# Kernel optimization log

Measured on AMD Instinct MI355X. Metric: run time of the kernel, lower is better.

## Reference

```python
import jax, jax.numpy as jnp
import numpy as np

B, S, H, NH = 2, 2048, 1024, 16
HD = H // NH  # 64
SCALE = HD ** -0.5


def setup_inputs() -> dict:
    key = jax.random.key(0)
    k1, k2, k3 = jax.random.split(key, 3)
    x = jax.random.normal(k1, (B, S, H), dtype=jnp.float32)
    w_qkv = jax.random.normal(k2, (H, 3 * H), dtype=jnp.float32) * (H ** -0.5)
    b_qkv = jnp.zeros((3 * H,), dtype=jnp.float32)
    w_out = jax.random.normal(k3, (H, H), dtype=jnp.float32) * (H ** -0.5)
    b_out = jnp.zeros((H,), dtype=jnp.float32)
    return {"x": x, "w_qkv": w_qkv, "b_qkv": b_qkv, "w_out": w_out, "b_out": b_out}


def reference(x, w_qkv, b_qkv, w_out, b_out):
    # qkv projection: [B,S,3H] -> split -> [B,NH,S,HD] each
    qkv = x @ w_qkv + b_qkv
    q, k, v = jnp.split(qkv, 3, axis=-1)
    def heads(t):
        return t.reshape(B, S, NH, HD).transpose(0, 2, 1, 3)  # [B,NH,S,HD]
    q, k, v = heads(q), heads(k), heads(v)
    # full (non-causal) softmax attention; chunking in the original is
    # math-equivalent since each query row attends over all keys
    scores = jnp.einsum('bhqd,bhkd->bhqk', q, k) * SCALE
    attn = jax.nn.softmax(scores, axis=-1)
    out = jnp.einsum('bhqk,bhkd->bhqd', attn, v)  # [B,NH,S,HD]
    out = out.transpose(0, 2, 1, 3).reshape(B, S, H)
    # to_out linear (Dropout is identity in eval mode)
    return out @ w_out + b_out
```

## Files before the change

### kernel.cpp

```cpp
#include <hip/hip_runtime.h>
#include <cstdint>

using u16 = unsigned short;
typedef __bf16 bf16x8 __attribute__((ext_vector_type(8)));
typedef __bf16 bf16x4 __attribute__((ext_vector_type(4)));
typedef float f32x4 __attribute__((ext_vector_type(4)));

#define MFMA16(a, b, c) __builtin_amdgcn_mfma_f32_16x16x32_bf16((a), (b), (c), 0, 0, 0)

__device__ __forceinline__ u16 f2bf(float f) {
  union { float f; uint32_t u; } c; c.f = f;
  uint32_t u = c.u;
  u += 0x7fffu + ((u >> 16) & 1u);
  return (u16)(u >> 16);
}

#if __has_builtin(__builtin_amdgcn_global_load_lds)
#define GLOAD_LDS16(g, l)                                                      \
  __builtin_amdgcn_global_load_lds(                                            \
      (__attribute__((address_space(1))) void*)(g),                            \
      (__attribute__((address_space(3))) void*)(l), 16, 0, 0)
#else
#define GLOAD_LDS16(g, l) do { *(uint4*)(l) = *(const uint4*)(g); } while (0)
#endif

__global__ __launch_bounds__(256) void prep(
    const float* __restrict__ x, const float* __restrict__ w_qkv,
    const float* __restrict__ w_out, u16* __restrict__ xb,
    u16* __restrict__ wqT, u16* __restrict__ woT) {
  const int bid = blockIdx.x, tid = threadIdx.x;
  if (bid < 4096) {
    int i = (bid * 256 + tid) * 4;
    float4 v = *(const float4*)&x[i];
    ushort4 p;
    p.x = f2bf(v.x); p.y = f2bf(v.y); p.z = f2bf(v.z); p.w = f2bf(v.w);
    *(ushort4*)&xb[i] = p;
    return;
  }
  __shared__ float tile[32][33];
  int t = bid - 4096;
  const float* in;
  u16* outp;
  int C, bx, by;
  if (t < 3072) { in = w_qkv; outp = wqT; C = 3072; bx = (t % 96) * 32; by = (t / 96) * 32; }
  else { t -= 3072; in = w_out; outp = woT; C = 1024; bx = (t % 32) * 32; by = (t / 32) * 32; }
  const int R = 1024;
  const int tx = tid & 31, ty = tid >> 5;
#pragma unroll
  for (int r2 = 0; r2 < 4; ++r2)
    tile[ty + r2 * 8][tx] = in[(size_t)(by + ty + r2 * 8) * C + bx + tx];
  __syncthreads();
#pragma unroll
  for (int r2 = 0; r2 < 4; ++r2)
    outp[(size_t)(bx + ty + r2 * 8) * R + by + tx] = f2bf(tile[tx][ty + r2 * 8]);
}

__global__ __launch_bounds__(256, 2) void gemm_qkv(
    const u16* __restrict__ A, const u16* __restrict__ Bt,
    const float* __restrict__ bias,
    u16* __restrict__ qb, u16* __restrict__ kb, u16* __restrict__ vb,
    int M, int N, int K) {
  __shared__ u16 As[128 * 32];
  __shared__ u16 Bs[128 * 32];
  const int tid = threadIdx.x;
  const int m0 = blockIdx.x * 128;
  const int n0 = blockIdx.y * 128;
  const int lane = tid & 63, w = tid >> 6;
  const int quad = lane >> 4, l16 = lane & 15;
  const int wr = w >> 1, wc = w & 1;

  f32x4 acc[4][4] = {};

  const int r0 = tid >> 2, p0 = tid & 3;
  const int r1 = r0 + 64;
  const int c8 = p0 ^ ((r0 >> 1) & 3);
  const u16* ga0 = A + (size_t)(m0 + r0) * K + c8 * 8;
  const u16* ga1 = A + (size_t)(m0 + r1) * K + c8 * 8;
  const u16* gb0 = Bt + (size_t)(n0 + r0) * K + c8 * 8;
  const u16* gb1 = Bt + (size_t)(n0 + r1) * K + c8 * 8;
  u16* la0 = &As[tid * 8];
  u16* la1 = &As[(tid + 256) * 8];
  u16* lb0 = &Bs[tid * 8];
  u16* lb1 = &Bs[(tid + 256) * 8];

  int aoff[4], boff[4];
#pragma unroll
  for (int i = 0; i < 4; ++i) {
    int ra = wr * 64 + i * 16 + l16;
    aoff[i] = (ra * 4 + (quad ^ ((ra >> 1) & 3))) * 8;
    int rb = wc * 64 + i * 16 + l16;
    boff[i] = (rb * 4 + (quad ^ ((rb >> 1) & 3))) * 8;
  }

  const int nIter = K >> 5;
  for (int kt = 0; kt < nIter; ++kt) {
    __syncthreads();
    const int kk = kt << 5;
    GLOAD_LDS16(ga0 + kk, la0);
    GLOAD_LDS16(ga1 + kk, la1);
    GLOAD_LDS16(gb0 + kk, lb0);
    GLOAD_LDS16(gb1 + kk, lb1);
    __syncthreads();
    bf16x8 af[4], bfr[4];
#pragma unroll
    for (int i = 0; i < 4; ++i) af[i] = *(const bf16x8*)&As[aoff[i]];
#pragma unroll
    for (int j = 0; j < 4; ++j) bfr[j] = *(const bf16x8*)&Bs[boff[j]];
#pragma unroll
    for (int i = 0; i < 4; ++i)
#pragma unroll
      for (int j = 0; j < 4; ++j)
        acc[i][j] = MFMA16(af[i], bfr[j], acc[i][j]);
  }

  const int S = 2048, NH = 16;
#pragma unroll
  for (int i = 0; i < 4; ++i) {
    const int mb = m0 + wr * 64 + i * 16 + quad * 4;
#pragma unroll
    for (int j = 0; j < 4; ++j) {
      const int n = n0 + wc * 64 + j * 16 + l16;
      const float bv = bias[n];
      const int which = n >> 10;
      const int hn = n & 1023;
      const int h = hn >> 6, d = hn & 63;
      const int b = mb >> 11, s = mb & 2047;
      const int bh = b * NH + h;
      if (which == 2) {
        ushort4 pk;
        pk.x = f2bf(acc[i][j][0] + bv);
        pk.y = f2bf(acc[i][j][1] + bv);
        pk.z = f2bf(acc[i][j][2] + bv);
        pk.w = f2bf(acc[i][j][3] + bv);
        *(ushort4*)&vb[((size_t)bh * 64 + d) * S + s] = pk;
      } else {
        const float sc = (which == 0) ? 0.18033688f : 1.0f;
        u16* dst = (which == 0) ? qb : kb;
#pragma unroll
        for (int r = 0; r < 4; ++r)
          dst[((size_t)bh * S + s + r) * 64 + d] = f2bf((acc[i][j][r] + bv) * sc);
      }
    }
  }
}

__global__ __launch_bounds__(256, 2) void gemm_out(
    const u16* __restrict__ A, const u16* __restrict__ Bt,
    const float* __restrict__ bias, float* __restrict__ outf,
    int M, int N, int K) {
  __shared__ u16 As[64 * 32];
  __shared__ u16 Bs[128 * 32];
  const int tid = threadIdx.x;
  const int m0 = blockIdx.x * 64;
  const int n0 = blockIdx.y * 128;
  const int lane = tid & 63, w = tid >> 6;
  const int quad = lane >> 4, l16 = lane & 15;
  const int wr = w >> 1, wc = w & 1;

  f32x4 acc[2][4] = {};

  const int r0 = tid >> 2, p0 = tid & 3;
  const int c8 = p0 ^ ((r0 >> 1) & 3);
  const u16* ga0 = A + (size_t)(m0 + r0) * K + c8 * 8;
  const u16* gb0 = Bt + (size_t)(n0 + r0) * K + c8 * 8;
  const u16* gb1 = Bt + (size_t)(n0 + r0 + 64) * K + c8 * 8;
  u16* la0 = &As[tid * 8];
  u16* lb0 = &Bs[tid * 8];
  u16* lb1 = &Bs[(tid + 256) * 8];

  int aoff[2], boff[4];
#pragma unroll
  for (int i = 0; i < 2; ++i) {
    int ra = wr * 32 + i * 16 + l16;
    aoff[i] = (ra * 4 + (quad ^ ((ra >> 1) & 3))) * 8;
  }
#pragma unroll
  for (int j = 0; j < 4; ++j) {
    int rb = wc * 64 + j * 16 + l16;
    boff[j] = (rb * 4 + (quad ^ ((rb >> 1) & 3))) * 8;
  }

  const int nIter = K >> 5;
  for (int kt = 0; kt < nIter; ++kt) {
    __syncthreads();
    const int kk = kt << 5;
    GLOAD_LDS16(ga0 + kk, la0);
    GLOAD_LDS16(gb0 + kk, lb0);
    GLOAD_LDS16(gb1 + kk, lb1);
    __syncthreads();
    bf16x8 af[2], bfr[4];
#pragma unroll
    for (int i = 0; i < 2; ++i) af[i] = *(const bf16x8*)&As[aoff[i]];
#pragma unroll
    for (int j = 0; j < 4; ++j) bfr[j] = *(const bf16x8*)&Bs[boff[j]];
#pragma unroll
    for (int i = 0; i < 2; ++i)
#pragma unroll
      for (int j = 0; j < 4; ++j)
        acc[i][j] = MFMA16(af[i], bfr[j], acc[i][j]);
  }

#pragma unroll
  for (int i = 0; i < 2; ++i) {
    const int mb = m0 + wr * 32 + i * 16 + quad * 4;
#pragma unroll
    for (int j = 0; j < 4; ++j) {
      const int n = n0 + wc * 64 + j * 16 + l16;
      const float bv = bias[n];
#pragma unroll
      for (int r = 0; r < 4; ++r)
        outf[(size_t)(mb + r) * N + n] = acc[i][j][r] + bv;
    }
  }
}

__global__ __launch_bounds__(128, 2) void attn_fa(
    const u16* __restrict__ qg, const u16* __restrict__ kg,
    const u16* __restrict__ vg, u16* __restrict__ o) {
  const int S = 2048, NH = 16;
  const int h = blockIdx.x, b = blockIdx.y, qblk = blockIdx.z;
  const int bh = b * NH + h;
  const int tid = threadIdx.x, w = tid >> 6, lane = tid & 63;
  const int quad = lane >> 4, l16 = lane & 15;

  __shared__ u16 Ks[2][4096];
  __shared__ u16 Vs[2][4096];
  __shared__ u16 Ps[2][4096];

  const int q0 = qblk * 128 + w * 64;

  bf16x8 qf[4][2];
#pragma unroll
  for (int qt = 0; qt < 4; ++qt) {
    const u16* qp = qg + ((size_t)bh * S + q0 + qt * 16 + l16) * 64 + quad * 8;
    qf[qt][0] = *(const bf16x8*)qp;
    qf[qt][1] = *(const bf16x8*)(qp + 32);
  }

  f32x4 accO[4][4] = {};
  f32x4 accL[4] = {};

  bf16x8 ones;
#pragma unroll
  for (int i = 0; i < 8; ++i) ones[i] = (__bf16)1.0f;

  const u16* kbase = kg + (size_t)bh * S * 64;
  const u16* vbase = vg + (size_t)bh * 64 * S;

  const int sr0 = tid >> 3, sp0 = tid & 7;
  const int c8s = sp0 ^ (sr0 & 7);
  const u16* kS[4];
  const u16* vS[4];
#pragma unroll
  for (int j = 0; j < 4; ++j) {
    kS[j] = kbase + (size_t)(sr0 + 16 * j) * 64 + c8s * 8;
    vS[j] = vbase + (size_t)(sr0 + 16 * j) * S + c8s * 8;
  }

  int koff[4][2];
#pragma unroll
  for (int ct = 0; ct < 4; ++ct) {
    int row = ct * 16 + l16;
    koff[ct][0] = (row * 8 + (quad ^ (row & 7))) * 8;
    koff[ct][1] = (row * 8 + ((quad + 4) ^ (row & 7))) * 8;
  }
  u16* Pw = Ps[w];
  int prow[4];
#pragma unroll
  for (int qt = 0; qt < 4; ++qt) prow[qt] = (qt * 16 + l16) * 64;
  int pgx[4];
#pragma unroll
  for (int ct = 0; ct < 4; ++ct) pgx[ct] = ((ct * 4 + quad) ^ l16) * 4;
  const int pr0 = ((quad * 2) ^ l16) * 4;

#pragma unroll
  for (int j = 0; j < 4; ++j) {
    GLOAD_LDS16(kS[j], &Ks[0][(tid + 128 * j) * 8]);
    GLOAD_LDS16(vS[j], &Vs[0][(tid + 128 * j) * 8]);
  }

  for (int kt = 0; kt < S / 64; ++kt) {
    const int cur = kt & 1;
    __syncthreads();
    if (kt + 1 < S / 64) {
      const int nb = cur ^ 1;
#pragma unroll
      for (int j = 0; j < 4; ++j) {
        GLOAD_LDS16(kS[j] + (size_t)(kt + 1) * 4096, &Ks[nb][(tid + 128 * j) * 8]);
        GLOAD_LDS16(vS[j] + (kt + 1) * 64, &Vs[nb][(tid + 128 * j) * 8]);
      }
    }
    const u16* Kc = Ks[cur];
    const u16* Vc = Vs[cur];

#pragma unroll
    for (int ct = 0; ct < 4; ++ct) {
      bf16x8 kf0 = *(const bf16x8*)&Kc[koff[ct][0]];
      bf16x8 kf1 = *(const bf16x8*)&Kc[koff[ct][1]];
      f32x4 s[4];
#pragma unroll
      for (int qt = 0; qt < 4; ++qt) {
        s[qt] = MFMA16(kf0, qf[qt][0], f32x4{});
        s[qt] = MFMA16(kf1, qf[qt][1], s[qt]);
      }
#pragma unroll
      for (int qt = 0; qt < 4; ++qt) {
#pragma unroll
        for (int r = 0; r < 4; ++r) s[qt][r] = __builtin_amdgcn_exp2f(s[qt][r]);
        bf16x4 pk = {(__bf16)s[qt][0], (__bf16)s[qt][1],
                     (__bf16)s[qt][2], (__bf16)s[qt][3]};
        *(bf16x4*)&Pw[prow[qt] + pgx[ct]] = pk;
      }
    }

    bf16x8 vf[4][2];
#pragma unroll
    for (int ct = 0; ct < 4; ++ct) {
      vf[ct][0] = *(const bf16x8*)&Vc[koff[ct][0]];
      vf[ct][1] = *(const bf16x8*)&Vc[koff[ct][1]];
    }

    bf16x8 pf[4][2];
#pragma unroll
    for (int qt = 0; qt < 4; ++qt) {
      bf16x4 t0 = *(const bf16x4*)&Pw[prow[qt] + pr0];
      bf16x4 t1 = *(const bf16x4*)&Pw[prow[qt] + (pr0 ^ 4)];
      bf16x4 t2 = *(const bf16x4*)&Pw[prow[qt] + (pr0 ^ 32)];
      bf16x4 t3 = *(const bf16x4*)&Pw[prow[qt] + (pr0 ^ 36)];
      pf[qt][0] = __builtin_shufflevector(t0, t1, 0, 1, 2, 3, 4, 5, 6, 7);
      pf[qt][1] = __builtin_shufflevector(t2, t3, 0, 1, 2, 3, 4, 5, 6, 7);
    }

#pragma unroll
    for (int qt = 0; qt < 4; ++qt) {
      accL[qt] = MFMA16(ones, pf[qt][0], accL[qt]);
      accL[qt] = MFMA16(ones, pf[qt][1], accL[qt]);
    }

#pragma unroll
    for (int ct = 0; ct < 4; ++ct)
#pragma unroll
      for (int qt = 0; qt < 4; ++qt) {
        accO[ct][qt] = MFMA16(vf[ct][0], pf[qt][0], accO[ct][qt]);
        accO[ct][qt] = MFMA16(vf[ct][1], pf[qt][1], accO[ct][qt]);
      }
  }

  float inv[4];
#pragma unroll
  for (int qt = 0; qt < 4; ++qt) inv[qt] = 1.f / accL[qt][0];

#pragma unroll
  for (int ct = 0; ct < 4; ++ct)
#pragma unroll
    for (int qt = 0; qt < 4; ++qt) {
      const int s = q0 + qt * 16 + l16;
      ushort4 pk;
      pk.x = f2bf(accO[ct][qt][0] * inv[qt]);
      pk.y = f2bf(accO[ct][qt][1] * inv[qt]);
      pk.z = f2bf(accO[ct][qt][2] * inv[qt]);
      pk.w = f2bf(accO[ct][qt][3] * inv[qt]);
      *(ushort4*)&o[(size_t)(b * S + s) * 1024 + h * 64 + ct * 16 + quad * 4] = pk;
    }
}


extern "C" void kernel_launch(void* const* d_in, const int* in_sizes, int n_in,
                              void* d_out, int out_size, void* d_ws, size_t ws_size,
                              hipStream_t stream) {
  const float* x = (const float*)d_in[0];
  const float* w_qkv = (const float*)d_in[1];
  const float* b_qkv = (const float*)d_in[2];
  const float* w_out = (const float*)d_in[3];
  const float* b_out = (const float*)d_in[4];
  float* out = (float*)d_out;

  u16* xb = (u16*)d_ws;
  u16* wqT = xb + 4096 * 1024;
  u16* woT = wqT + 3072 * 1024;
  u16* qb = woT + 1024 * 1024;
  u16* kb = qb + 4194304;
  u16* vb = kb + 4194304;
  u16* ao = vb + 4194304;

  prep<<<8192, 256, 0, stream>>>(x, w_qkv, w_out, xb, wqT, woT);
  gemm_qkv<<<dim3(32, 24), 256, 0, stream>>>(xb, wqT, b_qkv, qb, kb, vb,
                                             4096, 3072, 1024);
  attn_fa<<<dim3(16, 2, 16), 128, 0, stream>>>(qb, kb, vb, ao);
  gemm_out<<<dim3(64, 8), 256, 0, stream>>>(ao, woT, b_out, out,
                                            4096, 1024, 1024);
}
```

Before: 202.7 us.

## Split attention keys across four waves per query block with LDS reduction

The attention kernel now gives each block 64 queries and 4 waves. Each wave processes a disjoint quarter of the keys with its own double-buffered K LDS region and no block barriers in the main loop. V is loaded straight into registers from global memory rather than staged through LDS. Partial O and row sums are combined through a tree reduction in shared memory at the end. This doubles the grid and removes the per-tile __syncthreads, at the cost of an epilogue reduction and a tighter hand-written waitcnt pipeline.

```diff
diff --git a/kernel.cpp b/kernel.cpp
--- a/kernel.cpp
+++ b/kernel.cpp
@@ -214,7 +214,7 @@
   }
 }
 
-__global__ __launch_bounds__(128, 2) void attn_fa(
+__global__ __launch_bounds__(256, 2) void attn_fa(
     const u16* __restrict__ qg, const u16* __restrict__ kg,
     const u16* __restrict__ vg, u16* __restrict__ o) {
   const int S = 2048, NH = 16;
@@ -223,12 +223,12 @@
   const int tid = threadIdx.x, w = tid >> 6, lane = tid & 63;
   const int quad = lane >> 4, l16 = lane & 15;
 
-  __shared__ u16 Ks[2][4096];
-  __shared__ u16 Vs[2][4096];
-  __shared__ u16 Ps[2][4096];
-
-  const int q0 = qblk * 128 + w * 64;
-
+  __shared__ __align__(16) u16 smem[24576];
+  u16* Kw0 = smem + w * 2048;
+  u16* Kw1 = smem + 8192 + w * 2048;
+  u16* Pw  = smem + 16384 + w * 2048;
+
+  const int q0 = qblk * 64;
   bf16x8 qf[4][2];
 #pragma unroll
   for (int qt = 0; qt < 4; ++qt) {
@@ -237,131 +237,163 @@
     qf[qt][1] = *(const bf16x8*)(qp + 32);
   }
 
+  const u16* kbase = kg + (size_t)bh * S * 64;
+  const u16* vbase = vg + (size_t)bh * 64 * S;
+  const int key0w = w * 512;
+
+  const int sr = lane >> 3;
+  const int sc = (lane & 7) ^ sr;
+
+  int koff[2][2];
+#pragma unroll
+  for (int ct = 0; ct < 2; ++ct)
+#pragma unroll
+    for (int dh = 0; dh < 2; ++dh) {
+      int row = ct * 16 + l16;
+      koff[ct][dh] = (row * 8 + ((dh * 4 + quad) ^ (l16 & 7))) * 8;
+    }
+
+  const int swz = (l16 ^ (l16 >> 2)) & 3;
+  int pwA[4], pwB[4], prd[4];
+#pragma unroll
+  for (int qt = 0; qt < 4; ++qt) {
+    int rowb = (qt * 16 + l16) * 32;
+    pwA[qt] = rowb + (((quad >> 1) ^ swz)) * 8 + (quad & 1) * 4;
+    pwB[qt] = rowb + (((2 + (quad >> 1)) ^ swz)) * 8 + (quad & 1) * 4;
+    prd[qt] = rowb + ((quad ^ swz)) * 8;
+  }
+
   f32x4 accO[4][4] = {};
   f32x4 accL[4] = {};
-
   bf16x8 ones;
 #pragma unroll
   for (int i = 0; i < 8; ++i) ones[i] = (__bf16)1.0f;
 
-  const u16* kbase = kg + (size_t)bh * S * 64;
-  const u16* vbase = vg + (size_t)bh * 64 * S;
-
-  const int sr0 = tid >> 3, sp0 = tid & 7;
-  const int c8s = sp0 ^ (sr0 & 7);
-  const u16* kS[4];
-  const u16* vS[4];
-#pragma unroll
-  for (int j = 0; j < 4; ++j) {
-    kS[j] = kbase + (size_t)(sr0 + 16 * j) * 64 + c8s * 8;
-    vS[j] = vbase + (size_t)(sr0 + 16 * j) * S + c8s * 8;
-  }
-
-  int koff[4][2];
-#pragma unroll
-  for (int ct = 0; ct < 4; ++ct) {
-    int row = ct * 16 + l16;
-    koff[ct][0] = (row * 8 + (quad ^ (row & 7))) * 8;
-    koff[ct][1] = (row * 8 + ((quad + 4) ^ (row & 7))) * 8;
-  }
-  u16* Pw = Ps[w];
-  int prow[4];
-#pragma unroll
-  for (int qt = 0; qt < 4; ++qt) prow[qt] = (qt * 16 + l16) * 64;
-  int pgx[4];
-#pragma unroll
-  for (int ct = 0; ct < 4; ++ct) pgx[ct] = ((ct * 4 + quad) ^ l16) * 4;
-  const int pr0 = ((quad * 2) ^ l16) * 4;
-
-#pragma unroll
-  for (int j = 0; j < 4; ++j) {
-    GLOAD_LDS16(kS[j], &Ks[0][(tid + 128 * j) * 8]);
-    GLOAD_LDS16(vS[j], &Vs[0][(tid + 128 * j) * 8]);
-  }
-
-  for (int kt = 0; kt < S / 64; ++kt) {
-    const int cur = kt & 1;
-    __syncthreads();
-    if (kt + 1 < S / 64) {
-      const int nb = cur ^ 1;
-#pragma unroll
-      for (int j = 0; j < 4; ++j) {
-        GLOAD_LDS16(kS[j] + (size_t)(kt + 1) * 4096, &Ks[nb][(tid + 128 * j) * 8]);
-        GLOAD_LDS16(vS[j] + (kt + 1) * 64, &Vs[nb][(tid + 128 * j) * 8]);
+  bf16x8 vfA[4], vfB[4];
+
+  auto kdma = [&](int t, u16* BUF) {
+    const int kk = key0w + (t & 15) * 32;
+#pragma unroll
+    for (int j = 0; j < 4; ++j)
+      GLOAD_LDS16(kbase + (size_t)(kk + j * 8 + sr) * 64 + sc * 8,
+                  &BUF[j * 512 + lane * 8]);
+  };
+  auto vload = [&](int t, bf16x8 (&VF)[4]) {
+    const int kk = key0w + (t & 15) * 32;
+#pragma unroll
+    for (int ct = 0; ct < 4; ++ct)
+      VF[ct] = *(const bf16x8*)(vbase + (size_t)(ct * 16 + l16) * S + kk + quad * 8);
+  };
+  auto tile = [&](int t, u16* KBUF, bf16x8 (&VF)[4]) {
+    asm volatile("s_waitcnt vmcnt(8)" ::: "memory");
+    bf16x8 kf00 = *(const bf16x8*)&KBUF[koff[0][0]];
+    bf16x8 kf01 = *(const bf16x8*)&KBUF[koff[0][1]];
+    bf16x8 kf10 = *(const bf16x8*)&KBUF[koff[1][0]];
+    bf16x8 kf11 = *(const bf16x8*)&KBUF[koff[1][1]];
+    f32x4 s0[4], s1[4];
+    f32x4 z = {};
+#pragma unroll
+    for (int qt = 0; qt < 4; ++qt) {
+      s0[qt] = MFMA16(kf00, qf[qt][0], z);
+      s0[qt] = MFMA16(kf01, qf[qt][1], s0[qt]);
+      s1[qt] = MFMA16(kf10, qf[qt][0], z);
+      s1[qt] = MFMA16(kf11, qf[qt][1], s1[qt]);
+    }
+#pragma unroll
+    for (int qt = 0; qt < 4; ++qt)
+#pragma unroll
+      for (int r = 0; r < 4; ++r) {
+        s0[qt][r] = __builtin_amdgcn_exp2f(s0[qt][r]);
+        s1[qt][r] = __builtin_amdgcn_exp2f(s1[qt][r]);
       }
+#pragma unroll
+    for (int qt = 0; qt < 4; ++qt) {
+      bf16x4 a = {(__bf16)s0[qt][0], (__bf16)s0[qt][1],
+                  (__bf16)s0[qt][2], (__bf16)s0[qt][3]};
+      *(bf16x4*)&Pw[pwA[qt]] = a;
+      bf16x4 c = {(__bf16)s1[qt][0], (__bf16)s1[qt][1],
+                  (__bf16)s1[qt][2], (__bf16)s1[qt][3]};
+      *(bf16x4*)&Pw[pwB[qt]] = c;
     }
-    const u16* Kc = Ks[cur];
-    const u16* Vc = Vs[cur];
-
-#pragma unroll
-    for (int ct = 0; ct < 4; ++ct) {
-      bf16x8 kf0 = *(const bf16x8*)&Kc[koff[ct][0]];
-      bf16x8 kf1 = *(const bf16x8*)&Kc[koff[ct][1]];
-      f32x4 s[4];
+    bf16x8 pf[4];
+#pragma unroll
+    for (int qt = 0; qt < 4; ++qt) pf[qt] = *(const bf16x8*)&Pw[prd[qt]];
+#pragma unroll
+    for (int qt = 0; qt < 4; ++qt) accL[qt] = MFMA16(ones, pf[qt], accL[qt]);
+#pragma unroll
+    for (int ct = 0; ct < 4; ++ct)
+#pragma unroll
+      for (int qt = 0; qt < 4; ++qt)
+        accO[ct][qt] = MFMA16(VF[ct], pf[qt], accO[ct][qt]);
+    asm volatile("s_waitcnt lgkmcnt(0)" ::: "memory");
+    kdma(t + 2, KBUF);
+    vload(t + 2, VF);
+  };
+
+  kdma(0, Kw0); vload(0, vfA);
+  kdma(1, Kw1); vload(1, vfB);
+  for (int i = 0; i < 8; ++i) {
+    tile(2 * i, Kw0, vfA);
+    tile(2 * i + 1, Kw1, vfB);
+  }
+
+  f32x4 lv = {accL[0][0], accL[1][0], accL[2][0], accL[3][0]};
+  float* scr = (float*)smem;
+  __syncthreads();
+  if (w & 1) {
+    float* rb = scr + (w >> 1) * 4352;
+#pragma unroll
+    for (int ct = 0; ct < 4; ++ct)
+#pragma unroll
+      for (int qt = 0; qt < 4; ++qt)
+        *(f32x4*)&rb[((ct * 4 + qt) * 64 + lane) * 4] = accO[ct][qt];
+    *(f32x4*)&rb[(16 * 64 + lane) * 4] = lv;
+  }
+  __syncthreads();
+  if (!(w & 1)) {
+    float* rb = scr + (w >> 1) * 4352;
+#pragma unroll
+    for (int ct = 0; ct < 4; ++ct)
+#pragma unroll
+      for (int qt = 0; qt < 4; ++qt)
+        accO[ct][qt] += *(const f32x4*)&rb[((ct * 4 + qt) * 64 + lane) * 4];
+    lv += *(const f32x4*)&rb[(16 * 64 + lane) * 4];
+  }
+  __syncthreads();
+  if (w == 2) {
+    float* rb = scr;
+#pragma unroll
+    for (int ct = 0; ct < 4; ++ct)
+#pragma unroll
+      for (int qt = 0; qt < 4; ++qt)
+        *(f32x4*)&rb[((ct * 4 + qt) * 64 + lane) * 4] = accO[ct][qt];
+    *(f32x4*)&rb[(16 * 64 + lane) * 4] = lv;
+  }
+  __syncthreads();
+  if (w == 0) {
+    float* rb = scr;
+#pragma unroll
+    for (int ct = 0; ct < 4; ++ct)
+#pragma unroll
+      for (int qt = 0; qt < 4; ++qt)
+        accO[ct][qt] += *(const f32x4*)&rb[((ct * 4 + qt) * 64 + lane) * 4];
+    lv += *(const f32x4*)&rb[(16 * 64 + lane) * 4];
+    float inv[4];
+#pragma unroll
+    for (int qt = 0; qt < 4; ++qt) inv[qt] = 1.f / lv[qt];
+#pragma unroll
+    for (int ct = 0; ct < 4; ++ct)
 #pragma unroll
       for (int qt = 0; qt < 4; ++qt) {
-        s[qt] = MFMA16(kf0, qf[qt][0], f32x4{});
-        s[qt] = MFMA16(kf1, qf[qt][1], s[qt]);
+        const int s = q0 + qt * 16 + l16;
+        ushort4 pk;
+        pk.x = f2bf(accO[ct][qt][0] * inv[qt]);
+        pk.y = f2bf(accO[ct][qt][1] * inv[qt]);
+        pk.z = f2bf(accO[ct][qt][2] * inv[qt]);
+        pk.w = f2bf(accO[ct][qt][3] * inv[qt]);
+        *(ushort4*)&o[(size_t)(b * S + s) * 1024 + h * 64 + ct * 16 + quad * 4] = pk;
       }
-#pragma unroll
-      for (int qt = 0; qt < 4; ++qt) {
-#pragma unroll
-        for (int r = 0; r < 4; ++r) s[qt][r] = __builtin_amdgcn_exp2f(s[qt][r]);
-        bf16x4 pk = {(__bf16)s[qt][0], (__bf16)s[qt][1],
-                     (__bf16)s[qt][2], (__bf16)s[qt][3]};
-        *(bf16x4*)&Pw[prow[qt] + pgx[ct]] = pk;
-      }
-    }
-
-    bf16x8 vf[4][2];
-#pragma unroll
-    for (int ct = 0; ct < 4; ++ct) {
-      vf[ct][0] = *(const bf16x8*)&Vc[koff[ct][0]];
-      vf[ct][1] = *(const bf16x8*)&Vc[koff[ct][1]];
-    }
-
-    bf16x8 pf[4][2];
-#pragma unroll
-    for (int qt = 0; qt < 4; ++qt) {
-      bf16x4 t0 = *(const bf16x4*)&Pw[prow[qt] + pr0];
-      bf16x4 t1 = *(const bf16x4*)&Pw[prow[qt] + (pr0 ^ 4)];
-      bf16x4 t2 = *(const bf16x4*)&Pw[prow[qt] + (pr0 ^ 32)];
-      bf16x4 t3 = *(const bf16x4*)&Pw[prow[qt] + (pr0 ^ 36)];
-      pf[qt][0] = __builtin_shufflevector(t0, t1, 0, 1, 2, 3, 4, 5, 6, 7);
-      pf[qt][1] = __builtin_shufflevector(t2, t3, 0, 1, 2, 3, 4, 5, 6, 7);
-    }
-
-#pragma unroll
-    for (int qt = 0; qt < 4; ++qt) {
-      accL[qt] = MFMA16(ones, pf[qt][0], accL[qt]);
-      accL[qt] = MFMA16(ones, pf[qt][1], accL[qt]);
-    }
-
-#pragma unroll
-    for (int ct = 0; ct < 4; ++ct)
-#pragma unroll
-      for (int qt = 0; qt < 4; ++qt) {
-        accO[ct][qt] = MFMA16(vf[ct][0], pf[qt][0], accO[ct][qt]);
-        accO[ct][qt] = MFMA16(vf[ct][1], pf[qt][1], accO[ct][qt]);
-      }
-  }
-
-  float inv[4];
-#pragma unroll
-  for (int qt = 0; qt < 4; ++qt) inv[qt] = 1.f / accL[qt][0];
-
-#pragma unroll
-  for (int ct = 0; ct < 4; ++ct)
-#pragma unroll
-    for (int qt = 0; qt < 4; ++qt) {
-      const int s = q0 + qt * 16 + l16;
-      ushort4 pk;
-      pk.x = f2bf(accO[ct][qt][0] * inv[qt]);
-      pk.y = f2bf(accO[ct][qt][1] * inv[qt]);
-      pk.z = f2bf(accO[ct][qt][2] * inv[qt]);
-      pk.w = f2bf(accO[ct][qt][3] * inv[qt]);
-      *(ushort4*)&o[(size_t)(b * S + s) * 1024 + h * 64 + ct * 16 + quad * 4] = pk;
-    }
+  }
 }
 
 
@@ -386,7 +418,7 @@
   prep<<<8192, 256, 0, stream>>>(x, w_qkv, w_out, xb, wqT, woT);
   gemm_qkv<<<dim3(32, 24), 256, 0, stream>>>(xb, wqT, b_qkv, qb, kb, vb,
                                              4096, 3072, 1024);
-  attn_fa<<<dim3(16, 2, 16), 128, 0, stream>>>(qb, kb, vb, ao);
+  attn_fa<<<dim3(16, 2, 32), 256, 0, stream>>>(qb, kb, vb, ao);
   gemm_out<<<dim3(64, 8), 256, 0, stream>>>(ao, woT, b_out, out,
                                             4096, 1024, 1024);
 }
```

Result: faster. 187.2 us (-7.7%).
